# Kernel tuning notes

Hardware: AMD Instinct MI355X
Metric: run time of the kernel (lower is better)

Reference implementation:

```python
import jax, jax.numpy as jnp
import numpy as np


def _block_diag_mask(in4, out4):
    # mask[i*in:(i+1)*in, i*out:(i+1)*out] = 1 for i in 0..3; shape (4*in, 4*out)
    inp, out = in4 // 4, out4 // 4
    rows = jnp.arange(in4) // inp      # block id per input feature
    cols = jnp.arange(out4) // out     # block id per output feature
    return (rows[:, None] == cols[None, :]).astype(jnp.float32)


def setup_inputs() -> dict:
    key = jax.random.key(0)
    k1, k2, k3 = jax.random.split(key, 3)
    N, IN4, OUT4 = 8192, 2048, 2048
    x = jax.random.normal(k1, (N, IN4), dtype=jnp.float32)
    # weight stored as (4*output_dim, 4*input_dim), like torch nn.Linear
    W = jax.random.normal(k2, (OUT4, IN4), dtype=jnp.float32) * (1.0 / np.sqrt(IN4))
    b = jax.random.normal(k3, (OUT4,), dtype=jnp.float32) * 0.01
    return {"x": x, "W": W, "b": b}


def reference(x, W, b):
    out4, in4 = W.shape
    mask = _block_diag_mask(in4, out4)          # (4*in, 4*out)
    # original: input.matmul(weight.t() * mask) + bias
    masked_wt = W.T * mask                       # (4*in, 4*out)
    return x @ masked_wt + b
```

## Files before the change

### kernel.cpp

```cpp
#include <hip/hip_runtime.h>
#include <hip/hip_bf16.h>

typedef __attribute__((ext_vector_type(8))) short bf16x8;
typedef __attribute__((ext_vector_type(4))) float f32x4;

#define DIM  2048
#define GDIM 512
#define BM   128
#define BN   128
#define BK   32
#define NKT  16

__device__ __forceinline__ short f2bf(float f) {
  __bf16 h = (__bf16)f;
  return __builtin_bit_cast(short, h);
}

__device__ __forceinline__ void gload_lds16(const float* g, float* l) {
  __builtin_amdgcn_global_load_lds(
      (const __attribute__((address_space(1))) void*)g,
      (__attribute__((address_space(3))) void*)l, 16, 0, 0);
}

__global__ __launch_bounds__(512, 4)
void bdlinear_kernel(const float* __restrict__ X, const float* __restrict__ W,
                     const float* __restrict__ Bias, float* __restrict__ O) {
  __shared__ float ls[2][8192];

  int bid = blockIdx.x;
  bid = (bid & 7) * 128 + (bid >> 3);
  const int n_tile = bid & 15;
  const int m_tile = bid >> 4;
  const int g      = n_tile >> 2;
  const int row0   = m_tile * BM;
  const int col0   = n_tile * BN;
  const long k0    = (long)g * GDIM;

  const int t    = threadIdx.x;
  const int lane = t & 63;
  const int wid  = t >> 6;

  const int r    = lane >> 3;
  const int srcg = (lane & 7) ^ r;
  const float* gsrc[4];
  int ldoff[4];
  #pragma unroll
  for (int j = 0; j < 4; ++j) {
    const int seg = wid * 4 + j;
    ldoff[j] = seg * 256;
    if (seg < 16) {
      const int arow = seg * 8 + r;
      gsrc[j] = X + (size_t)(row0 + arow) * DIM + k0 + srcg * 4;
    } else {
      const int brow = (seg - 16) * 8 + r;
      gsrc[j] = W + (size_t)(col0 + brow) * DIM + k0 + srcg * 4;
    }
  }

  const int wm   = (wid & 1) * 64;
  const int wn   = (wid >> 1) * 32;
  const int lrow = lane & 15;
  const int lkb  = lane >> 4;

  f32x4 acc[4][2] = {};

  auto STAGE = [&](int buf, int kt) {
    #pragma unroll
    for (int j = 0; j < 4; ++j)
      gload_lds16(gsrc[j] + kt * BK, &ls[buf][ldoff[j]]);
  };

  STAGE(0, 0);
  __syncthreads();

  for (int kt = 0; kt < NKT; ++kt) {
    const int p = kt & 1;
    if (kt + 1 < NKT) STAGE(p ^ 1, kt + 1);

    bf16x8 af[4], bfr[2];
    #pragma unroll
    for (int mi = 0; mi < 4; ++mi) {
      const int row = wm + mi * 16 + lrow;
      const int s   = row & 7;
      const f32x4 a0 = *(const f32x4*)&ls[p][row * 32 + (((lkb * 2)     ^ s) * 4)];
      const f32x4 a1 = *(const f32x4*)&ls[p][row * 32 + (((lkb * 2 + 1) ^ s) * 4)];
      #pragma unroll
      for (int e = 0; e < 4; ++e) { af[mi][e] = f2bf(a0[e]); af[mi][4 + e] = f2bf(a1[e]); }
    }
    #pragma unroll
    for (int ni = 0; ni < 2; ++ni) {
      const int row = wn + ni * 16 + lrow;
      const int s   = row & 7;
      const f32x4 b0 = *(const f32x4*)&ls[p][4096 + row * 32 + (((lkb * 2)     ^ s) * 4)];
      const f32x4 b1 = *(const f32x4*)&ls[p][4096 + row * 32 + (((lkb * 2 + 1) ^ s) * 4)];
      #pragma unroll
      for (int e = 0; e < 4; ++e) { bfr[ni][e] = f2bf(b0[e]); bfr[ni][4 + e] = f2bf(b1[e]); }
    }
    #pragma unroll
    for (int mi = 0; mi < 4; ++mi)
      #pragma unroll
      for (int ni = 0; ni < 2; ++ni)
        acc[mi][ni] = __builtin_amdgcn_mfma_f32_16x16x32_bf16(
            af[mi], bfr[ni], acc[mi][ni], 0, 0, 0);

    __syncthreads();
  }

  #pragma unroll
  for (int ni = 0; ni < 2; ++ni) {
    const int ocol = col0 + wn + ni * 16 + lrow;
    const float bias = Bias[ocol];
    #pragma unroll
    for (int mi = 0; mi < 4; ++mi) {
      #pragma unroll
      for (int i = 0; i < 4; ++i) {
        const int orow = row0 + wm + mi * 16 + lkb * 4 + i;
        O[(size_t)orow * DIM + ocol] = acc[mi][ni][i] + bias;
      }
    }
  }
}

extern "C" void kernel_launch(void* const* d_in, const int* in_sizes, int n_in,
                              void* d_out, int out_size, void* d_ws, size_t ws_size,
                              hipStream_t stream) {
  const float* X = (const float*)d_in[0];
  const float* W = (const float*)d_in[1];
  const float* B = (const float*)d_in[2];
  float* O       = (float*)d_out;
  dim3 grid(64 * 16), block(512);
  hipLaunchKernelGGL(bdlinear_kernel, grid, block, 0, stream, X, W, B, O);
}
```

Baseline: 159.2 us.

## Pre-convert X and diagonal W blocks to bf16, then run bf16 GEMM

Adds a conversion kernel that writes X and the diagonal blocks of W as bf16 into workspace, then runs a GEMM that loads bf16 directly into LDS without per-tile conversion. The GEMM uses 256-thread blocks with larger 64x64 per-wave tiles and BK=64. This halves the bytes moved per tile and removes conversion ALU work from the inner loop, at the cost of an extra pass over X and an additional launch.

```diff
diff --git a/kernel.cpp b/kernel.cpp
--- a/kernel.cpp
+++ b/kernel.cpp
@@ -4,37 +4,61 @@
 typedef __attribute__((ext_vector_type(8))) short bf16x8;
 typedef __attribute__((ext_vector_type(4))) float f32x4;
 
-#define DIM  2048
-#define GDIM 512
-#define BM   128
-#define BN   128
-#define BK   32
-#define NKT  16
+#define DIM   2048
+#define GDIM  512
+#define NXCH  2097152
+#define NWCH  131072
+#define NTOT  (NXCH + NWCH)
 
 __device__ __forceinline__ short f2bf(float f) {
   __bf16 h = (__bf16)f;
   return __builtin_bit_cast(short, h);
 }
 
-__device__ __forceinline__ void gload_lds16(const float* g, float* l) {
+__device__ __forceinline__ void gload_lds16(const short* g, short* l) {
   __builtin_amdgcn_global_load_lds(
       (const __attribute__((address_space(1))) void*)g,
       (__attribute__((address_space(3))) void*)l, 16, 0, 0);
 }
 
-__global__ __launch_bounds__(512, 4)
-void bdlinear_kernel(const float* __restrict__ X, const float* __restrict__ W,
-                     const float* __restrict__ Bias, float* __restrict__ O) {
-  __shared__ float ls[2][8192];
+__global__ __launch_bounds__(256)
+void cvt_kernel(const float* __restrict__ X, const float* __restrict__ W,
+                short* __restrict__ Xbf, short* __restrict__ Wbf) {
+  const int stride = gridDim.x * blockDim.x;
+  for (int idx = blockIdx.x * blockDim.x + threadIdx.x; idx < NTOT; idx += stride) {
+    const float* src;
+    short* dst;
+    if (idx < NXCH) {
+      src = X + (size_t)idx * 8;
+      dst = Xbf + (size_t)idx * 8;
+    } else {
+      const int e = (idx - NXCH) * 8;
+      const int j = e >> 9;
+      const int k = e & 511;
+      src = W + (size_t)j * DIM + ((j >> 9) << 9) + k;
+      dst = Wbf + e;
+    }
+    const f32x4 a = ((const f32x4*)src)[0];
+    const f32x4 b = ((const f32x4*)src)[1];
+    bf16x8 o;
+    #pragma unroll
+    for (int e2 = 0; e2 < 4; ++e2) { o[e2] = f2bf(a[e2]); o[4 + e2] = f2bf(b[e2]); }
+    *(bf16x8*)dst = o;
+  }
+}
+
+__global__ __launch_bounds__(256, 2)
+void gemm_kernel(const short* __restrict__ Xbf, const short* __restrict__ Wbf,
+                 const float* __restrict__ Bias, float* __restrict__ O) {
+  __shared__ short ls[2][2][128][64];
 
   int bid = blockIdx.x;
   bid = (bid & 7) * 128 + (bid >> 3);
   const int n_tile = bid & 15;
   const int m_tile = bid >> 4;
   const int g      = n_tile >> 2;
-  const int row0   = m_tile * BM;
-  const int col0   = n_tile * BN;
-  const long k0    = (long)g * GDIM;
+  const int row0   = m_tile * 128;
+  const int col0   = n_tile * 128;
 
   const int t    = threadIdx.x;
   const int lane = t & 63;
@@ -42,72 +66,67 @@
 
   const int r    = lane >> 3;
   const int srcg = (lane & 7) ^ r;
-  const float* gsrc[4];
-  int ldoff[4];
+  const short* gA[4];
+  const short* gB[4];
+  short* dA[4];
+  short* dB[4];
   #pragma unroll
   for (int j = 0; j < 4; ++j) {
-    const int seg = wid * 4 + j;
-    ldoff[j] = seg * 256;
-    if (seg < 16) {
-      const int arow = seg * 8 + r;
-      gsrc[j] = X + (size_t)(row0 + arow) * DIM + k0 + srcg * 4;
-    } else {
-      const int brow = (seg - 16) * 8 + r;
-      gsrc[j] = W + (size_t)(col0 + brow) * DIM + k0 + srcg * 4;
-    }
+    const int s = wid * 4 + j;
+    gA[j] = Xbf + (size_t)(row0 + s * 8 + r) * DIM + g * GDIM + srcg * 8;
+    gB[j] = Wbf + (size_t)(col0 + s * 8 + r) * GDIM + srcg * 8;
+    dA[j] = &ls[0][0][s * 8][0];
+    dB[j] = &ls[0][1][s * 8][0];
   }
 
   const int wm   = (wid & 1) * 64;
-  const int wn   = (wid >> 1) * 32;
+  const int wn   = (wid >> 1) * 64;
   const int lrow = lane & 15;
   const int lkb  = lane >> 4;
 
-  f32x4 acc[4][2] = {};
+  f32x4 acc[4][4] = {};
 
   auto STAGE = [&](int buf, int kt) {
+    const int bo = buf * (2 * 128 * 64);
     #pragma unroll
-    for (int j = 0; j < 4; ++j)
-      gload_lds16(gsrc[j] + kt * BK, &ls[buf][ldoff[j]]);
+    for (int j = 0; j < 4; ++j) {
+      gload_lds16(gA[j] + kt * 64, dA[j] + bo);
+      gload_lds16(gB[j] + kt * 64, dB[j] + bo);
+    }
   };
 
   STAGE(0, 0);
   __syncthreads();
 
-  for (int kt = 0; kt < NKT; ++kt) {
+  for (int kt = 0; kt < 8; ++kt) {
     const int p = kt & 1;
-    if (kt + 1 < NKT) STAGE(p ^ 1, kt + 1);
+    if (kt + 1 < 8) STAGE(p ^ 1, kt + 1);
 
-    bf16x8 af[4], bfr[2];
     #pragma unroll
-    for (int mi = 0; mi < 4; ++mi) {
-      const int row = wm + mi * 16 + lrow;
-      const int s   = row & 7;
-      const f32x4 a0 = *(const f32x4*)&ls[p][row * 32 + (((lkb * 2)     ^ s) * 4)];
-      const f32x4 a1 = *(const f32x4*)&ls[p][row * 32 + (((lkb * 2 + 1) ^ s) * 4)];
+    for (int ks = 0; ks < 2; ++ks) {
+      bf16x8 af[4], bfr[4];
       #pragma unroll
-      for (int e = 0; e < 4; ++e) { af[mi][e] = f2bf(a0[e]); af[mi][4 + e] = f2bf(a1[e]); }
+      for (int mi = 0; mi < 4; ++mi) {
+        const int row = wm + mi * 16 + lrow;
+        af[mi] = *(const bf16x8*)&ls[p][0][row][(((ks * 4 + lkb) ^ (row & 7)) * 8)];
+      }
+      #pragma unroll
+      for (int ni = 0; ni < 4; ++ni) {
+        const int row = wn + ni * 16 + lrow;
+        bfr[ni] = *(const bf16x8*)&ls[p][1][row][(((ks * 4 + lkb) ^ (row & 7)) * 8)];
+      }
+      #pragma unroll
+      for (int mi = 0; mi < 4; ++mi)
+        #pragma unroll
+        for (int ni = 0; ni < 4; ++ni)
+          acc[mi][ni] = __builtin_amdgcn_mfma_f32_16x16x32_bf16(
+              af[mi], bfr[ni], acc[mi][ni], 0, 0, 0);
     }
-    #pragma unroll
-    for (int ni = 0; ni < 2; ++ni) {
-      const int row = wn + ni * 16 + lrow;
-      const int s   = row & 7;
-      const f32x4 b0 = *(const f32x4*)&ls[p][4096 + row * 32 + (((lkb * 2)     ^ s) * 4)];
-      const f32x4 b1 = *(const f32x4*)&ls[p][4096 + row * 32 + (((lkb * 2 + 1) ^ s) * 4)];
-      #pragma unroll
-      for (int e = 0; e < 4; ++e) { bfr[ni][e] = f2bf(b0[e]); bfr[ni][4 + e] = f2bf(b1[e]); }
-    }
-    #pragma unroll
-    for (int mi = 0; mi < 4; ++mi)
-      #pragma unroll
-      for (int ni = 0; ni < 2; ++ni)
-        acc[mi][ni] = __builtin_amdgcn_mfma_f32_16x16x32_bf16(
-            af[mi], bfr[ni], acc[mi][ni], 0, 0, 0);
-
     __syncthreads();
   }
 
   #pragma unroll
-  for (int ni = 0; ni < 2; ++ni) {
+  for (int ni = 0; ni < 4; ++ni) {
     const int ocol = col0 + wn + ni * 16 + lrow;
     const float bias = Bias[ocol];
     #pragma unroll
@@ -128,6 +147,9 @@
   const float* W = (const float*)d_in[1];
   const float* B = (const float*)d_in[2];
   float* O       = (float*)d_out;
-  dim3 grid(64 * 16), block(512);
-  hipLaunchKernelGGL(bdlinear_kernel, grid, block, 0, stream, X, W, B, O);
+  short* Xbf     = (short*)d_ws;
+  short* Wbf     = Xbf + (size_t)8192 * 2048;
+
+  hipLaunchKernelGGL(cvt_kernel, dim3(2048), dim3(256), 0, stream, X, W, Xbf, Wbf);
+  hipLaunchKernelGGL(gemm_kernel, dim3(1024), dim3(256), 0, stream, Xbf, Wbf, B, O);
 }
```

Result: faster. 145.4 us (-8.7%).
